# Kernel optimization log

Measured on AMD Instinct MI355X. Metric: run time of the kernel, lower is better.

Reference implementation:

```python
import jax, jax.numpy as jnp
import numpy as np

N_NODES = 50000
N_EDGES = 800000
D_IN = 128
D_HID = 128
D_OUT = 128


def setup_inputs() -> dict:
    key = jax.random.key(0)
    ks = jax.random.split(key, 5)
    x = jax.random.normal(ks[0], (N_NODES, D_IN), dtype=jnp.float32)
    edge_index = jax.random.randint(ks[1], (2, N_EDGES), 0, N_NODES, dtype=jnp.int64)
    # Glorot-ish init for the two GCN linear weights (PyG uses glorot)
    W1 = jax.random.normal(ks[2], (D_IN, D_HID), dtype=jnp.float32) * (1.0 / np.sqrt(D_IN))
    b1 = jnp.zeros((D_HID,), dtype=jnp.float32)
    W2 = jax.random.normal(ks[3], (D_HID, D_OUT), dtype=jnp.float32) * (1.0 / np.sqrt(D_HID))
    b2 = jnp.zeros((D_OUT,), dtype=jnp.float32)
    return {"x": x, "edge_index": edge_index, "W1": W1, "b1": b1, "W2": W2, "b2": b2}


def _gcn_layer(x, W, b, src, dst, dinv):
    """PyG GCNConv: h = xW; out[j] = sum_{(i->j)} dinv[i]*dinv[j]*h[i] + dinv[j]^2*h[j] (self-loop) + b."""
    n = x.shape[0]
    h = x @ W                                   # [N, D_out]
    coef = (dinv[src] * dinv[dst])[:, None]     # [E, 1] symmetric norm
    msg = h[src] * coef                         # [E, D_out] gather + scale
    agg = jax.ops.segment_sum(msg, dst, num_segments=n)  # scatter-add
    agg = agg + h * (dinv * dinv)[:, None]      # self-loop contribution
    return agg + b


def reference(x, edge_index, W1, b1, W2, b2):
    src = edge_index[0]
    dst = edge_index[1]
    n = x.shape[0]
    # degree over target nodes, including the added self-loop (+1)
    deg = jax.ops.segment_sum(jnp.ones_like(dst, dtype=x.dtype), dst, num_segments=n) + 1.0
    dinv = jax.lax.rsqrt(deg)
    h = jax.nn.relu(_gcn_layer(x, W1, b1, src, dst, dinv))
    return _gcn_layer(h, W2, b2, src, dst, dinv)
```

## Files before the change

### kernel.cpp

```cpp
#include <hip/hip_runtime.h>
#include <hip/hip_fp16.h>

#define NN 50000
#define NE 800000
#define D 128
#define NBLK ((NN + 255) / 256)

typedef __attribute__((ext_vector_type(8))) short bf16x8;
typedef __attribute__((ext_vector_type(4))) float f32x4;

static __device__ __forceinline__ unsigned short f2bf(float f) {
    unsigned u = __builtin_bit_cast(unsigned, f);
    unsigned r = (u + 0x7fffu + ((u >> 16) & 1u)) >> 16;
    return (unsigned short)r;
}
static __device__ __forceinline__ float bf2f(unsigned short h) {
    unsigned u = ((unsigned)h) << 16;
    return __builtin_bit_cast(float, u);
}

__global__ __launch_bounds__(256) void k_zero_cnt(int* __restrict__ cnt) {
    int i = blockIdx.x * 256 + threadIdx.x;
    if (i < NN) cnt[i] = 0;
}

__global__ __launch_bounds__(256) void k_count(const int* __restrict__ dst, int* __restrict__ cnt) {
    int e = blockIdx.x * 256 + threadIdx.x;
    if (e < NE) atomicAdd(&cnt[dst[e]], 1);
}

__global__ __launch_bounds__(256) void k_scan_partial(const int* __restrict__ cnt, int* __restrict__ blockSums) {
    __shared__ int s[256];
    int t = threadIdx.x;
    int i = blockIdx.x * 256 + t;
    s[t] = (i < NN) ? cnt[i] : 0;
    __syncthreads();
    for (int off = 128; off > 0; off >>= 1) {
        if (t < off) s[t] += s[t + off];
        __syncthreads();
    }
    if (t == 0) blockSums[blockIdx.x] = s[0];
}

__global__ __launch_bounds__(256) void k_scan_blocks(int* __restrict__ blockSums, int* __restrict__ row_ptr) {
    __shared__ int s[256];
    int t = threadIdx.x;
    int v = (t < NBLK) ? blockSums[t] : 0;
    s[t] = v;
    __syncthreads();
    for (int off = 1; off < 256; off <<= 1) {
        int y = (t >= off) ? s[t - off] : 0;
        __syncthreads();
        s[t] += y;
        __syncthreads();
    }
    if (t < NBLK) blockSums[t] = s[t] - v;
    if (t == 0) row_ptr[NN] = NE;
}

__global__ __launch_bounds__(256) void k_scan_final(const int* __restrict__ cnt, const int* __restrict__ blockOffs,
                                                    int* __restrict__ row_ptr, int* __restrict__ cursor,
                                                    float* __restrict__ dinv) {
    __shared__ int s[256];
    int t = threadIdx.x;
    int i = blockIdx.x * 256 + t;
    int v = (i < NN) ? cnt[i] : 0;
    s[t] = v;
    __syncthreads();
    for (int off = 1; off < 256; off <<= 1) {
        int y = (t >= off) ? s[t - off] : 0;
        __syncthreads();
        s[t] += y;
        __syncthreads();
    }
    if (i < NN) {
        int excl = s[t] - v + blockOffs[blockIdx.x];
        row_ptr[i] = excl;
        cursor[i] = excl;
        dinv[i] = rsqrtf((float)v + 1.0f);
    }
}

__global__ __launch_bounds__(256) void k_fill(const int* __restrict__ src, const int* __restrict__ dst,
                                              int* __restrict__ cursor, unsigned short* __restrict__ csr) {
    int e = blockIdx.x * 256 + threadIdx.x;
    if (e < NE) {
        int pos = atomicAdd(&cursor[dst[e]], 1);
        csr[pos] = (unsigned short)src[e];
    }
}

__global__ __launch_bounds__(256) void k_prepw(const float* __restrict__ W1, const float* __restrict__ W2,
                                               char* __restrict__ img1, char* __restrict__ img2) {
    int b = blockIdx.x;
    const float* W = (b < 64) ? W1 : W2;
    char* img = (b < 64) ? img1 : img2;
    int e = (b & 63) * 256 + threadIdx.x;
    int k = e >> 7, n = e & 127;
    float f = W[e];
    unsigned short hi = f2bf(f);
    float rem = f - bf2f(hi);
    unsigned short lo = f2bf(rem);
    unsigned off = (unsigned)((n << 8) + (k << 1)) ^ (unsigned)((n & 7) << 4);
    *(unsigned short*)(img + off) = hi;
    *(unsigned short*)(img + 32768 + off) = lo;
}

template <bool RELU_IN>
__global__ __launch_bounds__(256) void k_mgemm(const float* __restrict__ A, const char* __restrict__ wimg,
                                               __half* __restrict__ H) {
    __shared__ char lds[65536];
    const int t = threadIdx.x;

    {
        const float4* gv = (const float4*)wimg;
        float4* lv = (float4*)lds;
#pragma unroll
        for (int i = 0; i < 16; ++i) lv[i * 256 + t] = gv[i * 256 + t];
    }
    __syncthreads();

    const int lane = t & 63;
    const int wv = t >> 6;
    const int r0 = blockIdx.x * 64 + wv * 16;
    const int rl = lane & 15;
    const int g = lane >> 4;
    int arow = r0 + rl;
    if (arow >= NN) arow = NN - 1;
    const float* ar = A + (size_t)arow * D + g * 8;

    f32x4 acc[8];
#pragma unroll
    for (int j = 0; j < 8; ++j) acc[j] = (f32x4){0.f, 0.f, 0.f, 0.f};

#pragma unroll
    for (int ks = 0; ks < 4; ++ks) {
        float av[8];
        float4 p0 = *(const float4*)(ar + ks * 32);
        float4 p1 = *(const float4*)(ar + ks * 32 + 4);
        av[0] = p0.x; av[1] = p0.y; av[2] = p0.z; av[3] = p0.w;
        av[4] = p1.x; av[5] = p1.y; av[6] = p1.z; av[7] = p1.w;
        bf16x8 ah, al;
#pragma unroll
        for (int i = 0; i < 8; ++i) {
            float a = RELU_IN ? fmaxf(av[i], 0.f) : av[i];
            unsigned short h = f2bf(a);
            ah[i] = (short)h;
            al[i] = (short)f2bf(a - bf2f(h));
        }
        const int kofs = (ks * 32 + g * 8) << 1;
#pragma unroll
        for (int j = 0; j < 8; ++j) {
            int n = j * 16 + rl;
            unsigned off = (unsigned)((n << 8) + kofs) ^ (unsigned)((n & 7) << 4);
            bf16x8 bh = *(const bf16x8*)(lds + off);
            bf16x8 bl = *(const bf16x8*)(lds + 32768 + off);
            acc[j] = __builtin_amdgcn_mfma_f32_16x16x32_bf16(ah, bh, acc[j], 0, 0, 0);
            acc[j] = __builtin_amdgcn_mfma_f32_16x16x32_bf16(ah, bl, acc[j], 0, 0, 0);
            acc[j] = __builtin_amdgcn_mfma_f32_16x16x32_bf16(al, bh, acc[j], 0, 0, 0);
        }
    }

#pragma unroll
    for (int j = 0; j < 8; ++j) {
#pragma unroll
        for (int i = 0; i < 4; ++i) {
            int row = r0 + g * 4 + i;
            if (row < NN) H[(size_t)row * D + j * 16 + rl] = __float2half(acc[j][i]);
        }
    }
}

__global__ __launch_bounds__(256) void k_pull(const __half* __restrict__ H, const float* __restrict__ dinv,
                                              const float* __restrict__ b, const int* __restrict__ row_ptr,
                                              const unsigned short* __restrict__ csr, float* __restrict__ out) {
    int wid = (blockIdx.x * 256 + threadIdx.x) >> 6;
    int lane = threadIdx.x & 63;
    int node = __builtin_amdgcn_readfirstlane(wid);
    int rl = lane & 15;
    int g = lane >> 4;

    float dd = dinv[node];

    float2 a0 = {0.f, 0.f}, a1 = {0.f, 0.f}, a2 = {0.f, 0.f}, a3 = {0.f, 0.f};

    int beg = row_ptr[node];
    int end = row_ptr[node + 1];
    for (int i = beg + g; i < end; i += 4) {
        int s = csr[i];
        float c = dinv[s] * dd;
        float4 raw = *(const float4*)(H + (size_t)s * D + rl * 8);
        const __half2* hh = (const __half2*)&raw;
        float2 f0 = __half22float2(hh[0]);
        float2 f1 = __half22float2(hh[1]);
        float2 f2 = __half22float2(hh[2]);
        float2 f3 = __half22float2(hh[3]);
        a0.x = fmaf(f0.x, c, a0.x); a0.y = fmaf(f0.y, c, a0.y);
        a1.x = fmaf(f1.x, c, a1.x); a1.y = fmaf(f1.y, c, a1.y);
        a2.x = fmaf(f2.x, c, a2.x); a2.y = fmaf(f2.y, c, a2.y);
        a3.x = fmaf(f3.x, c, a3.x); a3.y = fmaf(f3.y, c, a3.y);
    }

    float v[8] = {a0.x, a0.y, a1.x, a1.y, a2.x, a2.y, a3.x, a3.y};
#pragma unroll
    for (int i = 0; i < 8; ++i) {
        v[i] += __shfl_xor(v[i], 16);
        v[i] += __shfl_xor(v[i], 32);
    }

    if (g == 0) {
        float s2 = dd * dd;
        float4 raw = *(const float4*)(H + (size_t)node * D + rl * 8);
        const __half2* hh = (const __half2*)&raw;
        float2 s0 = __half22float2(hh[0]);
        float2 s1 = __half22float2(hh[1]);
        float2 s2v = __half22float2(hh[2]);
        float2 s3 = __half22float2(hh[3]);
        float4 b0 = ((const float4*)b)[rl * 2];
        float4 b1 = ((const float4*)b)[rl * 2 + 1];
        float4 r0, r1;
        r0.x = fmaf(s0.x, s2, v[0] + b0.x);
        r0.y = fmaf(s0.y, s2, v[1] + b0.y);
        r0.z = fmaf(s1.x, s2, v[2] + b0.z);
        r0.w = fmaf(s1.y, s2, v[3] + b0.w);
        r1.x = fmaf(s2v.x, s2, v[4] + b1.x);
        r1.y = fmaf(s2v.y, s2, v[5] + b1.y);
        r1.z = fmaf(s3.x, s2, v[6] + b1.z);
        r1.w = fmaf(s3.y, s2, v[7] + b1.w);
        float4* op = (float4*)(out + (size_t)node * D + rl * 8);
        op[0] = r0;
        op[1] = r1;
    }
}

extern "C" void kernel_launch(void* const* d_in, const int* in_sizes, int n_in,
                              void* d_out, int out_size, void* d_ws, size_t ws_size,
                              hipStream_t stream) {
    const float* x  = (const float*)d_in[0];
    const int*   ei = (const int*)d_in[1];
    const float* W1 = (const float*)d_in[2];
    const float* b1 = (const float*)d_in[3];
    const float* W2 = (const float*)d_in[4];
    const float* b2 = (const float*)d_in[5];
    float* out = (float*)d_out;

    const int* src = ei;
    const int* dst = ei + NE;

    char* ws = (char*)d_ws;
    int*    cnt       = (int*)   (ws + 0);
    int*    row_ptr   = (int*)   (ws + 204800);
    int*    cursor    = (int*)   (ws + 409600);
    int*    blockSums = (int*)   (ws + 614400);
    float*  dinv      = (float*) (ws + 615424);
    char*   wimg1     = (char*)  (ws + 819200);
    char*   wimg2     = (char*)  (ws + 884736);
    unsigned short* csr = (unsigned short*)(ws + 950272);
    __half* h         = (__half*)(ws + 2550784);

    const int nBlkEdge = (NE + 255) / 256;
    const int nBlkGemm = (NN + 63) / 64;
    const int nBlkPull = NN / 4;

    k_zero_cnt<<<NBLK, 256, 0, stream>>>(cnt);
    k_count<<<nBlkEdge, 256, 0, stream>>>(dst, cnt);
    k_scan_partial<<<NBLK, 256, 0, stream>>>(cnt, blockSums);
    k_scan_blocks<<<1, 256, 0, stream>>>(blockSums, row_ptr);
    k_scan_final<<<NBLK, 256, 0, stream>>>(cnt, blockSums, row_ptr, cursor, dinv);
    k_fill<<<nBlkEdge, 256, 0, stream>>>(src, dst, cursor, csr);
    k_prepw<<<128, 256, 0, stream>>>(W1, W2, wimg1, wimg2);

    k_mgemm<false><<<nBlkGemm, 256, 0, stream>>>(x, wimg1, h);
    k_pull<<<nBlkPull, 256, 0, stream>>>(h, dinv, b1, row_ptr, csr, out);

    k_mgemm<true><<<nBlkGemm, 256, 0, stream>>>(out, wimg2, h);
    k_pull<<<nBlkPull, 256, 0, stream>>>(h, dinv, b2, row_ptr, csr, out);
}
```

Before: 267.2 us.

## Record per-edge rank during counting to drop fill atomics; unroll pull loop by two

The count kernel now saves the atomicAdd return value as each edge's rank, so the fill kernel can place edges at row_ptr[dst]+rank without a second round of atomics on a cursor array. This removes the cursor array but adds a 3.2 MB rank buffer that is written and then read back. Separately, the pull loop handles two neighbours per iteration with independent accumulators, so more gather loads are in flight at once, at the cost of extra registers.

```diff
diff --git a/kernel.cpp b/kernel.cpp
--- a/kernel.cpp
+++ b/kernel.cpp
@@ -24,9 +24,10 @@
     if (i < NN) cnt[i] = 0;
 }
 
-__global__ __launch_bounds__(256) void k_count(const int* __restrict__ dst, int* __restrict__ cnt) {
+__global__ __launch_bounds__(256) void k_count(const int* __restrict__ dst, int* __restrict__ cnt,
+                                               int* __restrict__ rank) {
     int e = blockIdx.x * 256 + threadIdx.x;
-    if (e < NE) atomicAdd(&cnt[dst[e]], 1);
+    if (e < NE) rank[e] = atomicAdd(&cnt[dst[e]], 1);
 }
 
 __global__ __launch_bounds__(256) void k_scan_partial(const int* __restrict__ cnt, int* __restrict__ blockSums) {
@@ -59,8 +60,7 @@
 }
 
 __global__ __launch_bounds__(256) void k_scan_final(const int* __restrict__ cnt, const int* __restrict__ blockOffs,
-                                                    int* __restrict__ row_ptr, int* __restrict__ cursor,
-                                                    float* __restrict__ dinv) {
+                                                    int* __restrict__ row_ptr, float* __restrict__ dinv) {
     __shared__ int s[256];
     int t = threadIdx.x;
     int i = blockIdx.x * 256 + t;
@@ -74,19 +74,18 @@
         __syncthreads();
     }
     if (i < NN) {
-        int excl = s[t] - v + blockOffs[blockIdx.x];
-        row_ptr[i] = excl;
-        cursor[i] = excl;
+        row_ptr[i] = s[t] - v + blockOffs[blockIdx.x];
         dinv[i] = rsqrtf((float)v + 1.0f);
     }
 }
 
 __global__ __launch_bounds__(256) void k_fill(const int* __restrict__ src, const int* __restrict__ dst,
-                                              int* __restrict__ cursor, unsigned short* __restrict__ csr) {
+                                              const int* __restrict__ rank, const int* __restrict__ row_ptr,
+                                              unsigned short* __restrict__ csr) {
     int e = blockIdx.x * 256 + threadIdx.x;
     if (e < NE) {
-        int pos = atomicAdd(&cursor[dst[e]], 1);
-        csr[pos] = (unsigned short)src[e];
+        int d = dst[e];
+        csr[row_ptr[d] + rank[e]] = (unsigned short)src[e];
     }
 }
 
@@ -183,23 +182,42 @@
     float dd = dinv[node];
 
     float2 a0 = {0.f, 0.f}, a1 = {0.f, 0.f}, a2 = {0.f, 0.f}, a3 = {0.f, 0.f};
+    float2 c0b = {0.f, 0.f}, c1b = {0.f, 0.f}, c2b = {0.f, 0.f}, c3b = {0.f, 0.f};
 
     int beg = row_ptr[node];
     int end = row_ptr[node + 1];
-    for (int i = beg + g; i < end; i += 4) {
-        int s = csr[i];
-        float c = dinv[s] * dd;
-        float4 raw = *(const float4*)(H + (size_t)s * D + rl * 8);
-        const __half2* hh = (const __half2*)&raw;
-        float2 f0 = __half22float2(hh[0]);
-        float2 f1 = __half22float2(hh[1]);
-        float2 f2 = __half22float2(hh[2]);
-        float2 f3 = __half22float2(hh[3]);
-        a0.x = fmaf(f0.x, c, a0.x); a0.y = fmaf(f0.y, c, a0.y);
-        a1.x = fmaf(f1.x, c, a1.x); a1.y = fmaf(f1.y, c, a1.y);
-        a2.x = fmaf(f2.x, c, a2.x); a2.y = fmaf(f2.y, c, a2.y);
-        a3.x = fmaf(f3.x, c, a3.x); a3.y = fmaf(f3.y, c, a3.y);
-    }
+    for (int i = beg + g; i < end; i += 8) {
+        int i1 = i + 4;
+        bool ok = i1 < end;
+        int s0 = csr[i];
+        int s1 = csr[ok ? i1 : i];
+        float c0 = dinv[s0] * dd;
+        float c1 = ok ? dinv[s1] * dd : 0.f;
+        float4 raw0 = *(const float4*)(H + (size_t)s0 * D + rl * 8);
+        float4 raw1 = *(const float4*)(H + (size_t)s1 * D + rl * 8);
+        const __half2* h0 = (const __half2*)&raw0;
+        const __half2* h1 = (const __half2*)&raw1;
+        float2 f0 = __half22float2(h0[0]);
+        float2 f1 = __half22float2(h0[1]);
+        float2 f2 = __half22float2(h0[2]);
+        float2 f3 = __half22float2(h0[3]);
+        a0.x = fmaf(f0.x, c0, a0.x); a0.y = fmaf(f0.y, c0, a0.y);
+        a1.x = fmaf(f1.x, c0, a1.x); a1.y = fmaf(f1.y, c0, a1.y);
+        a2.x = fmaf(f2.x, c0, a2.x); a2.y = fmaf(f2.y, c0, a2.y);
+        a3.x = fmaf(f3.x, c0, a3.x); a3.y = fmaf(f3.y, c0, a3.y);
+        float2 g0 = __half22float2(h1[0]);
+        float2 g1 = __half22float2(h1[1]);
+        float2 g2 = __half22float2(h1[2]);
+        float2 g3 = __half22float2(h1[3]);
+        c0b.x = fmaf(g0.x, c1, c0b.x); c0b.y = fmaf(g0.y, c1, c0b.y);
+        c1b.x = fmaf(g1.x, c1, c1b.x); c1b.y = fmaf(g1.y, c1, c1b.y);
+        c2b.x = fmaf(g2.x, c1, c2b.x); c2b.y = fmaf(g2.y, c1, c2b.y);
+        c3b.x = fmaf(g3.x, c1, c3b.x); c3b.y = fmaf(g3.y, c1, c3b.y);
+    }
+    a0.x += c0b.x; a0.y += c0b.y;
+    a1.x += c1b.x; a1.y += c1b.y;
+    a2.x += c2b.x; a2.y += c2b.y;
+    a3.x += c3b.x; a3.y += c3b.y;
 
     float v[8] = {a0.x, a0.y, a1.x, a1.y, a2.x, a2.y, a3.x, a3.y};
 #pragma unroll
@@ -250,24 +268,24 @@
     char* ws = (char*)d_ws;
     int*    cnt       = (int*)   (ws + 0);
     int*    row_ptr   = (int*)   (ws + 204800);
-    int*    cursor    = (int*)   (ws + 409600);
-    int*    blockSums = (int*)   (ws + 614400);
-    float*  dinv      = (float*) (ws + 615424);
-    char*   wimg1     = (char*)  (ws + 819200);
-    char*   wimg2     = (char*)  (ws + 884736);
-    unsigned short* csr = (unsigned short*)(ws + 950272);
-    __half* h         = (__half*)(ws + 2550784);
+    int*    blockSums = (int*)   (ws + 409600);
+    float*  dinv      = (float*) (ws + 410624);
+    char*   wimg1     = (char*)  (ws + 614400);
+    char*   wimg2     = (char*)  (ws + 679936);
+    int*    rank      = (int*)   (ws + 745472);
+    unsigned short* csr = (unsigned short*)(ws + 3945472);
+    __half* h         = (__half*)(ws + 5545472);
 
     const int nBlkEdge = (NE + 255) / 256;
     const int nBlkGemm = (NN + 63) / 64;
     const int nBlkPull = NN / 4;
 
     k_zero_cnt<<<NBLK, 256, 0, stream>>>(cnt);
-    k_count<<<nBlkEdge, 256, 0, stream>>>(dst, cnt);
+    k_count<<<nBlkEdge, 256, 0, stream>>>(dst, cnt, rank);
     k_scan_partial<<<NBLK, 256, 0, stream>>>(cnt, blockSums);
     k_scan_blocks<<<1, 256, 0, stream>>>(blockSums, row_ptr);
-    k_scan_final<<<NBLK, 256, 0, stream>>>(cnt, blockSums, row_ptr, cursor, dinv);
-    k_fill<<<nBlkEdge, 256, 0, stream>>>(src, dst, cursor, csr);
+    k_scan_final<<<NBLK, 256, 0, stream>>>(cnt, blockSums, row_ptr, dinv);
+    k_fill<<<nBlkEdge, 256, 0, stream>>>(src, dst, rank, row_ptr, csr);
     k_prepw<<<128, 256, 0, stream>>>(W1, W2, wimg1, wimg2);
 
     k_mgemm<false><<<nBlkGemm, 256, 0, stream>>>(x, wimg1, h);
```

Result: faster. 238.3 us (-10.8%).

## Split features into column-quarter planes, store hidden in fp16, precompute CSR ranks

Applied to the files above, without the earlier changes.

The hidden activations H are stored as four planes of 32 columns each, so each pull wave aggregates one quarter of a node's features, with 16 edges in flight per wave. The layer-1 output is written as fp16 in the same plane layout and read directly by the second GEMM. The CSR build records each edge's atomic rank while counting, so the fill pass needs no second atomic, and the zero kernel becomes a memset. The intent is less gather traffic per plane and smaller intermediates, at the cost of four times as many waves and fp16 rounding of the hidden layer.

```diff
diff --git a/kernel.cpp b/kernel.cpp
--- a/kernel.cpp
+++ b/kernel.cpp
@@ -19,14 +19,10 @@
     return __builtin_bit_cast(float, u);
 }
 
-__global__ __launch_bounds__(256) void k_zero_cnt(int* __restrict__ cnt) {
-    int i = blockIdx.x * 256 + threadIdx.x;
-    if (i < NN) cnt[i] = 0;
-}
-
-__global__ __launch_bounds__(256) void k_count(const int* __restrict__ dst, int* __restrict__ cnt) {
+__global__ __launch_bounds__(256) void k_count(const int* __restrict__ dst, int* __restrict__ cnt,
+                                               int* __restrict__ rank) {
     int e = blockIdx.x * 256 + threadIdx.x;
-    if (e < NE) atomicAdd(&cnt[dst[e]], 1);
+    if (e < NE) rank[e] = atomicAdd(&cnt[dst[e]], 1);
 }
 
 __global__ __launch_bounds__(256) void k_scan_partial(const int* __restrict__ cnt, int* __restrict__ blockSums) {
@@ -59,8 +55,7 @@
 }
 
 __global__ __launch_bounds__(256) void k_scan_final(const int* __restrict__ cnt, const int* __restrict__ blockOffs,
-                                                    int* __restrict__ row_ptr, int* __restrict__ cursor,
-                                                    float* __restrict__ dinv) {
+                                                    int* __restrict__ row_ptr, float* __restrict__ dinv) {
     __shared__ int s[256];
     int t = threadIdx.x;
     int i = blockIdx.x * 256 + t;
@@ -74,19 +69,18 @@
         __syncthreads();
     }
     if (i < NN) {
-        int excl = s[t] - v + blockOffs[blockIdx.x];
-        row_ptr[i] = excl;
-        cursor[i] = excl;
+        row_ptr[i] = s[t] - v + blockOffs[blockIdx.x];
         dinv[i] = rsqrtf((float)v + 1.0f);
     }
 }
 
 __global__ __launch_bounds__(256) void k_fill(const int* __restrict__ src, const int* __restrict__ dst,
-                                              int* __restrict__ cursor, unsigned short* __restrict__ csr) {
+                                              const int* __restrict__ rank, const int* __restrict__ row_ptr,
+                                              unsigned short* __restrict__ csr) {
     int e = blockIdx.x * 256 + threadIdx.x;
     if (e < NE) {
-        int pos = atomicAdd(&cursor[dst[e]], 1);
-        csr[pos] = (unsigned short)src[e];
+        int d = dst[e];
+        csr[row_ptr[d] + rank[e]] = (unsigned short)src[e];
     }
 }
 
@@ -106,8 +100,8 @@
     *(unsigned short*)(img + 32768 + off) = lo;
 }
 
-template <bool RELU_IN>
-__global__ __launch_bounds__(256) void k_mgemm(const float* __restrict__ A, const char* __restrict__ wimg,
+template <bool RELU_IN, bool A_FP16>
+__global__ __launch_bounds__(256) void k_mgemm(const void* __restrict__ Av, const char* __restrict__ wimg,
                                                __half* __restrict__ H) {
     __shared__ char lds[65536];
     const int t = threadIdx.x;
@@ -127,7 +121,6 @@
     const int g = lane >> 4;
     int arow = r0 + rl;
     if (arow >= NN) arow = NN - 1;
-    const float* ar = A + (size_t)arow * D + g * 8;
 
     f32x4 acc[8];
 #pragma unroll
@@ -136,10 +129,25 @@
 #pragma unroll
     for (int ks = 0; ks < 4; ++ks) {
         float av[8];
-        float4 p0 = *(const float4*)(ar + ks * 32);
-        float4 p1 = *(const float4*)(ar + ks * 32 + 4);
-        av[0] = p0.x; av[1] = p0.y; av[2] = p0.z; av[3] = p0.w;
-        av[4] = p1.x; av[5] = p1.y; av[6] = p1.z; av[7] = p1.w;
+        if (A_FP16) {
+            const __half* A = (const __half*)Av;
+            const __half* ap = A + (size_t)ks * (NN * 32) + (size_t)arow * 32 + g * 8;
+            float4 raw = *(const float4*)ap;
+            const __half2* hh = (const __half2*)&raw;
+            float2 t0 = __half22float2(hh[0]);
+            float2 t1 = __half22float2(hh[1]);
+            float2 t2 = __half22float2(hh[2]);
+            float2 t3 = __half22float2(hh[3]);
+            av[0] = t0.x; av[1] = t0.y; av[2] = t1.x; av[3] = t1.y;
+            av[4] = t2.x; av[5] = t2.y; av[6] = t3.x; av[7] = t3.y;
+        } else {
+            const float* A = (const float*)Av;
+            const float* ar = A + (size_t)arow * D + g * 8 + ks * 32;
+            float4 p0 = *(const float4*)ar;
+            float4 p1 = *(const float4*)(ar + 4);
+            av[0] = p0.x; av[1] = p0.y; av[2] = p0.z; av[3] = p0.w;
+            av[4] = p1.x; av[5] = p1.y; av[6] = p1.z; av[7] = p1.w;
+        }
         bf16x8 ah, al;
 #pragma unroll
         for (int i = 0; i < 8; ++i) {
@@ -163,33 +171,38 @@
 
 #pragma unroll
     for (int j = 0; j < 8; ++j) {
+        const int qq = j >> 1;
+        const int cq = (j & 1) * 16 + rl;
 #pragma unroll
         for (int i = 0; i < 4; ++i) {
             int row = r0 + g * 4 + i;
-            if (row < NN) H[(size_t)row * D + j * 16 + rl] = __float2half(acc[j][i]);
-        }
-    }
-}
-
+            if (row < NN) H[(size_t)qq * (NN * 32) + (size_t)row * 32 + cq] = __float2half(acc[j][i]);
+        }
+    }
+}
+
+template <bool OUT_FP16>
 __global__ __launch_bounds__(256) void k_pull(const __half* __restrict__ H, const float* __restrict__ dinv,
                                               const float* __restrict__ b, const int* __restrict__ row_ptr,
-                                              const unsigned short* __restrict__ csr, float* __restrict__ out) {
+                                              const unsigned short* __restrict__ csr, void* __restrict__ outv) {
     int wid = (blockIdx.x * 256 + threadIdx.x) >> 6;
     int lane = threadIdx.x & 63;
-    int node = __builtin_amdgcn_readfirstlane(wid);
-    int rl = lane & 15;
-    int g = lane >> 4;
-
+    int node = __builtin_amdgcn_readfirstlane(wid >> 2);
+    int q = __builtin_amdgcn_readfirstlane(wid & 3);
+    int rl = lane & 3;
+    int g = lane >> 2;
+
+    const __half* Hq = H + (size_t)q * (NN * 32);
     float dd = dinv[node];
 
     float2 a0 = {0.f, 0.f}, a1 = {0.f, 0.f}, a2 = {0.f, 0.f}, a3 = {0.f, 0.f};
 
     int beg = row_ptr[node];
     int end = row_ptr[node + 1];
-    for (int i = beg + g; i < end; i += 4) {
+    for (int i = beg + g; i < end; i += 16) {
         int s = csr[i];
         float c = dinv[s] * dd;
-        float4 raw = *(const float4*)(H + (size_t)s * D + rl * 8);
+        float4 raw = *(const float4*)(Hq + (size_t)s * 32 + rl * 8);
         const __half2* hh = (const __half2*)&raw;
         float2 f0 = __half22float2(hh[0]);
         float2 f1 = __half22float2(hh[1]);
@@ -204,32 +217,46 @@
     float v[8] = {a0.x, a0.y, a1.x, a1.y, a2.x, a2.y, a3.x, a3.y};
 #pragma unroll
     for (int i = 0; i < 8; ++i) {
+        v[i] += __shfl_xor(v[i], 4);
+        v[i] += __shfl_xor(v[i], 8);
         v[i] += __shfl_xor(v[i], 16);
         v[i] += __shfl_xor(v[i], 32);
     }
 
     if (g == 0) {
         float s2 = dd * dd;
-        float4 raw = *(const float4*)(H + (size_t)node * D + rl * 8);
+        float4 raw = *(const float4*)(Hq + (size_t)node * 32 + rl * 8);
         const __half2* hh = (const __half2*)&raw;
         float2 s0 = __half22float2(hh[0]);
         float2 s1 = __half22float2(hh[1]);
         float2 s2v = __half22float2(hh[2]);
         float2 s3 = __half22float2(hh[3]);
-        float4 b0 = ((const float4*)b)[rl * 2];
-        float4 b1 = ((const float4*)b)[rl * 2 + 1];
-        float4 r0, r1;
-        r0.x = fmaf(s0.x, s2, v[0] + b0.x);
-        r0.y = fmaf(s0.y, s2, v[1] + b0.y);
-        r0.z = fmaf(s1.x, s2, v[2] + b0.z);
-        r0.w = fmaf(s1.y, s2, v[3] + b0.w);
-        r1.x = fmaf(s2v.x, s2, v[4] + b1.x);
-        r1.y = fmaf(s2v.y, s2, v[5] + b1.y);
-        r1.z = fmaf(s3.x, s2, v[6] + b1.z);
-        r1.w = fmaf(s3.y, s2, v[7] + b1.w);
-        float4* op = (float4*)(out + (size_t)node * D + rl * 8);
-        op[0] = r0;
-        op[1] = r1;
+        const float* bq = b + q * 32 + rl * 8;
+        float4 b0 = *(const float4*)bq;
+        float4 b1v = *(const float4*)(bq + 4);
+        float r[8];
+        r[0] = fmaf(s0.x, s2, v[0] + b0.x);
+        r[1] = fmaf(s0.y, s2, v[1] + b0.y);
+        r[2] = fmaf(s1.x, s2, v[2] + b0.z);
+        r[3] = fmaf(s1.y, s2, v[3] + b0.w);
+        r[4] = fmaf(s2v.x, s2, v[4] + b1v.x);
+        r[5] = fmaf(s2v.y, s2, v[5] + b1v.y);
+        r[6] = fmaf(s3.x, s2, v[6] + b1v.z);
+        r[7] = fmaf(s3.y, s2, v[7] + b1v.w);
+        if (OUT_FP16) {
+            __half* out = (__half*)outv;
+            __half2 o[4];
+            o[0] = __floats2half2_rn(r[0], r[1]);
+            o[1] = __floats2half2_rn(r[2], r[3]);
+            o[2] = __floats2half2_rn(r[4], r[5]);
+            o[3] = __floats2half2_rn(r[6], r[7]);
+            *(float4*)(out + (size_t)q * (NN * 32) + (size_t)node * 32 + rl * 8) = *(float4*)o;
+        } else {
+            float* out = (float*)outv;
+            float* op = out + (size_t)node * D + q * 32 + rl * 8;
+            *(float4*)op = make_float4(r[0], r[1], r[2], r[3]);
+            *(float4*)(op + 4) = make_float4(r[4], r[5], r[6], r[7]);
+        }
     }
 }
 
@@ -250,29 +277,30 @@
     char* ws = (char*)d_ws;
     int*    cnt       = (int*)   (ws + 0);
     int*    row_ptr   = (int*)   (ws + 204800);
-    int*    cursor    = (int*)   (ws + 409600);
-    int*    blockSums = (int*)   (ws + 614400);
-    float*  dinv      = (float*) (ws + 615424);
-    char*   wimg1     = (char*)  (ws + 819200);
-    char*   wimg2     = (char*)  (ws + 884736);
-    unsigned short* csr = (unsigned short*)(ws + 950272);
-    __half* h         = (__half*)(ws + 2550784);
+    int*    blockSums = (int*)   (ws + 409600);
+    float*  dinv      = (float*) (ws + 410624);
+    char*   wimg1     = (char*)  (ws + 614400);
+    char*   wimg2     = (char*)  (ws + 679936);
+    int*    rank      = (int*)   (ws + 745472);
+    unsigned short* csr = (unsigned short*)(ws + 3945472);
+    __half* h         = (__half*)(ws + 5545472);
+    __half* h2        = (__half*)(ws + 18345472);
 
     const int nBlkEdge = (NE + 255) / 256;
     const int nBlkGemm = (NN + 63) / 64;
-    const int nBlkPull = NN / 4;
-
-    k_zero_cnt<<<NBLK, 256, 0, stream>>>(cnt);
-    k_count<<<nBlkEdge, 256, 0, stream>>>(dst, cnt);
+    const int nBlkPull = NN;
+
+    hipMemsetAsync(cnt, 0, (size_t)NN * 4, stream);
+    k_count<<<nBlkEdge, 256, 0, stream>>>(dst, cnt, rank);
     k_scan_partial<<<NBLK, 256, 0, stream>>>(cnt, blockSums);
     k_scan_blocks<<<1, 256, 0, stream>>>(blockSums, row_ptr);
-    k_scan_final<<<NBLK, 256, 0, stream>>>(cnt, blockSums, row_ptr, cursor, dinv);
-    k_fill<<<nBlkEdge, 256, 0, stream>>>(src, dst, cursor, csr);
+    k_scan_final<<<NBLK, 256, 0, stream>>>(cnt, blockSums, row_ptr, dinv);
+    k_fill<<<nBlkEdge, 256, 0, stream>>>(src, dst, rank, row_ptr, csr);
     k_prepw<<<128, 256, 0, stream>>>(W1, W2, wimg1, wimg2);
 
-    k_mgemm<false><<<nBlkGemm, 256, 0, stream>>>(x, wimg1, h);
-    k_pull<<<nBlkPull, 256, 0, stream>>>(h, dinv, b1, row_ptr, csr, out);
-
-    k_mgemm<true><<<nBlkGemm, 256, 0, stream>>>(out, wimg2, h);
-    k_pull<<<nBlkPull, 256, 0, stream>>>(h, dinv, b2, row_ptr, csr, out);
-}
+    k_mgemm<false, false><<<nBlkGemm, 256, 0, stream>>>(x, wimg1, h);
+    k_pull<true><<<nBlkPull, 256, 0, stream>>>(h, dinv, b1, row_ptr, csr, h2);
+
+    k_mgemm<true, true><<<nBlkGemm, 256, 0, stream>>>(h2, wimg2, h);
+    k_pull<false><<<nBlkPull, 256, 0, stream>>>(h, dinv, b2, row_ptr, csr, out);
+}
```

Measured after the change: 315.5 us. 1.18x slower.
